# Kernel tuning notes

Hardware: AMD Instinct MI355X
Metric: run time of the kernel (lower is better)

Reference implementation:

```python
import jax, jax.numpy as jnp
import numpy as np

DIM = 1024
HEADS = 16
HEAD_DIM = DIM // HEADS
SCALE = HEAD_DIM ** -0.5
B, N = 2, 2048


def setup_inputs() -> dict:
    key = jax.random.key(0)
    ks = jax.random.split(key, 12)
    s = DIM ** -0.5
    return {
        "x_real": jax.random.normal(ks[0], (B, N, DIM), jnp.float32),
        "x_imag": jax.random.normal(ks[1], (B, N, DIM), jnp.float32),
        "Wqkv_r": jax.random.normal(ks[2], (3 * DIM, DIM), jnp.float32) * s,
        "bqkv_r": jax.random.normal(ks[3], (3 * DIM,), jnp.float32) * 0.01,
        "Wqkv_i": jax.random.normal(ks[4], (3 * DIM, DIM), jnp.float32) * s,
        "bqkv_i": jax.random.normal(ks[5], (3 * DIM,), jnp.float32) * 0.01,
        "Wout_r": jax.random.normal(ks[6], (DIM, DIM), jnp.float32) * s,
        "bout_r": jax.random.normal(ks[7], (DIM,), jnp.float32) * 0.01,
        "Wout_i": jax.random.normal(ks[8], (DIM, DIM), jnp.float32) * s,
        "bout_i": jax.random.normal(ks[9], (DIM,), jnp.float32) * 0.01,
    }


def _split_heads(qkv):
    # (B, N, 3*D) -> q, k, v each (B, H, N, hd)
    b, n, _ = qkv.shape
    qkv = qkv.reshape(b, n, 3, HEADS, HEAD_DIM).transpose(2, 0, 3, 1, 4)
    return qkv[0], qkv[1], qkv[2]


def reference(x_real, x_imag, Wqkv_r, bqkv_r, Wqkv_i, bqkv_i,
              Wout_r, bout_r, Wout_i, bout_i):
    b, n, d = x_real.shape
    q_r, k_r, v_r = _split_heads(x_real @ Wqkv_r.T + bqkv_r)
    q_i, k_i, v_i = _split_heads(x_imag @ Wqkv_i.T + bqkv_i)

    # complex score: (q_r + i q_i) (k_r - i k_i)^T pattern per source
    attn_real = (jnp.einsum('bhqd,bhkd->bhqk', q_r, k_r)
                 + jnp.einsum('bhqd,bhkd->bhqk', q_i, k_i)) * SCALE
    attn_imag = (jnp.einsum('bhqd,bhkd->bhqk', q_i, k_r)
                 - jnp.einsum('bhqd,bhkd->bhqk', q_r, k_i)) * SCALE
    attn_mag = jnp.sqrt(attn_real ** 2 + attn_imag ** 2)
    w = jax.nn.softmax(attn_mag, axis=-1)

    out_r = jnp.einsum('bhqk,bhkd->bhqd', w, v_r).transpose(0, 2, 1, 3).reshape(b, n, d)
    out_i = jnp.einsum('bhqk,bhkd->bhqd', w, v_i).transpose(0, 2, 1, 3).reshape(b, n, d)
    out_r = out_r @ Wout_r.T + bout_r
    out_i = out_i @ Wout_i.T + bout_i
    return out_r, out_i
```

## Files before the change

kernel.cpp:

```cpp
#include <hip/hip_runtime.h>


#define DIM_   1024
#define HEADS_ 16
#define HD_    64
#define BB_    2
#define NN_    2048
#define MTOT_  (BB_*NN_)
#define SCALE_ 0.125f

typedef __bf16 bf16;
typedef __bf16 bf16x8 __attribute__((ext_vector_type(8)));
typedef short  s16x8  __attribute__((ext_vector_type(8)));
typedef float  fx4    __attribute__((ext_vector_type(4)));

__device__ __forceinline__ bf16x8 neg8(bf16x8 v) {
    s16x8 s;
    __builtin_memcpy(&s, &v, sizeof(s));
    s ^= (short)0x8000;
    bf16x8 r;
    __builtin_memcpy(&r, &s, sizeof(r));
    return r;
}

__device__ __forceinline__ void gl_lds16(const void* g, void* l) {
    __builtin_amdgcn_global_load_lds(
        (const __attribute__((address_space(1))) unsigned int*)g,
        (__attribute__((address_space(3))) unsigned int*)l, 16, 0, 0);
}

#define PIPE_SYNC() asm volatile("s_waitcnt vmcnt(2)\n\ts_barrier" ::: "memory")

__global__ __launch_bounds__(256) void cvt_prepass(
    const float* __restrict__ xr, const float* __restrict__ xi,
    const float* __restrict__ wqr, const float* __restrict__ wqi,
    const float* __restrict__ wor, const float* __restrict__ woi,
    bf16* __restrict__ xbf, bf16* __restrict__ wqkv, bf16* __restrict__ wout)
{
    const int bid = blockIdx.x;
    const float* src; bf16* dst; int rel;
    if      (bid < 2048) { src = xr;  dst = xbf;           rel = bid; }
    else if (bid < 4096) { src = xi;  dst = xbf + 4194304; rel = bid - 2048; }
    else if (bid < 5632) { src = wqr; dst = wqkv;          rel = bid - 4096; }
    else if (bid < 7168) { src = wqi; dst = wqkv + 3145728; rel = bid - 5632; }
    else if (bid < 7680) { src = wor; dst = wout;          rel = bid - 7168; }
    else                 { src = woi; dst = wout + 1048576; rel = bid - 7680; }
    size_t base = (size_t)rel * 2048 + (size_t)threadIdx.x * 8;
    fx4 a = *(const fx4*)(src + base);
    fx4 b = *(const fx4*)(src + base + 4);
    bf16x8 o;
#pragma unroll
    for (int j = 0; j < 4; ++j) { o[j] = (bf16)a[j]; o[j+4] = (bf16)b[j]; }
    *(bf16x8*)(dst + base) = o;
}

#define GEMM_CORE(Aptr, Bptr)                                                  \
    __shared__ __align__(16) bf16 As[128*64];                                  \
    __shared__ __align__(16) bf16 Bs[128*64];                                  \
    const int tid  = threadIdx.x;                                              \
    const int w    = tid >> 6, lane = tid & 63;                                \
    const int quad = lane >> 4, lc = lane & 15;                                \
    const int wm   = (w >> 1) * 64, wn = (w & 1) * 64;                         \
    const int rj   = lane >> 3;                                                \
    const int sc   = (lane & 7) ^ rj;                                          \
    const fx4 fzero = {0.f, 0.f, 0.f, 0.f};                                    \
    fx4 acc[4][4];                                                             \
    _Pragma("unroll")                                                          \
    for (int mi = 0; mi < 4; ++mi)                                             \
        _Pragma("unroll")                                                      \
        for (int ni = 0; ni < 4; ++ni) acc[mi][ni] = fzero;                    \
    for (int k0 = 0; k0 < DIM_; k0 += 64) {                                    \
        _Pragma("unroll")                                                      \
        for (int j = 0; j < 4; ++j) {                                          \
            int grp = j*4 + w;                                                 \
            int gr  = grp*8 + rj;                                              \
            gl_lds16(Aptr + (size_t)(m0+gr)*DIM_ + k0 + sc*8, As + grp*512);   \
            gl_lds16(Bptr + (size_t)(n0+gr)*DIM_ + k0 + sc*8, Bs + grp*512);   \
        }                                                                      \
        __syncthreads();                                                       \
        bf16x8 af[2][4], bfr[2][4];                                            \
        _Pragma("unroll")                                                      \
        for (int ks = 0; ks < 2; ++ks) {                                       \
            _Pragma("unroll")                                                  \
            for (int mi = 0; mi < 4; ++mi)                                     \
                af[ks][mi] = *(bf16x8*)&As[(wm+mi*16+lc)*64 + (((ks*4+quad)^(lc&7))*8)]; \
            _Pragma("unroll")                                                  \
            for (int ni = 0; ni < 4; ++ni)                                     \
                bfr[ks][ni] = *(bf16x8*)&Bs[(wn+ni*16+lc)*64 + (((ks*4+quad)^(lc&7))*8)]; \
        }                                                                      \
        _Pragma("unroll")                                                      \
        for (int ks = 0; ks < 2; ++ks)                                         \
            _Pragma("unroll")                                                  \
            for (int mi = 0; mi < 4; ++mi)                                     \
                _Pragma("unroll")                                              \
                for (int ni = 0; ni < 4; ++ni)                                 \
                    acc[mi][ni] = __builtin_amdgcn_mfma_f32_16x16x32_bf16(     \
                        af[ks][mi], bfr[ks][ni], acc[mi][ni], 0, 0, 0);        \
        __syncthreads();                                                       \
    }

__global__ __launch_bounds__(256) void qkv_gemm_dma(
    const bf16* __restrict__ xbf, const bf16* __restrict__ wqkv,
    const float* __restrict__ br, const float* __restrict__ bi,
    bf16* __restrict__ qbuf, bf16* __restrict__ kbuf, bf16* __restrict__ vbuf)
{
    const int z = blockIdx.z;
    const bf16* __restrict__ Ap = xbf  + (size_t)z * 4194304;
    const bf16* __restrict__ Bp = wqkv + (size_t)z * 3145728;
    const float* __restrict__ bias = z ? bi : br;
    const int n0 = blockIdx.x * 128;
    const int m0 = blockIdx.y * 128;

    GEMM_CORE(Ap, Bp)

#pragma unroll
    for (int mi = 0; mi < 4; ++mi)
#pragma unroll
        for (int ni = 0; ni < 4; ++ni)
#pragma unroll
            for (int r = 0; r < 4; ++r) {
                int gm = m0 + wm + mi*16 + quad*4 + r;
                int gc = n0 + wn + ni*16 + lc;
                float val = acc[mi][ni][r] + bias[gc];
                bf16 bv = (bf16)val;
                int which = gc >> 10, h = (gc >> 6) & 15, hd = gc & 63;
                int b = gm >> 11, n = gm & 2047;
                size_t base = (size_t)((z*BB_ + b)*HEADS_ + h);
                if (which == 0)      qbuf[(base*NN_ + n)*HD_ + hd] = bv;
                else if (which == 1) kbuf[(base*NN_ + n)*HD_ + hd] = bv;
                else                 vbuf[(base*HD_ + hd)*NN_ + n] = bv;
            }
}

__global__ __launch_bounds__(256) void out_gemm_dma(
    const bf16* __restrict__ obuf, const bf16* __restrict__ wout,
    const float* __restrict__ br, const float* __restrict__ bi,
    float* __restrict__ out)
{
    const int z = blockIdx.z;
    const bf16* __restrict__ Ap = obuf + (size_t)z * 4194304;
    const bf16* __restrict__ Bp = wout + (size_t)z * 1048576;
    const float* __restrict__ bias = z ? bi : br;
    float* __restrict__ dst = out + (size_t)z * 4194304;
    const int n0 = blockIdx.x * 128;
    const int m0 = blockIdx.y * 128;

    GEMM_CORE(Ap, Bp)

#pragma unroll
    for (int mi = 0; mi < 4; ++mi)
#pragma unroll
        for (int ni = 0; ni < 4; ++ni)
#pragma unroll
            for (int r = 0; r < 4; ++r) {
                int gm = m0 + wm + mi*16 + quad*4 + r;
                int gc = n0 + wn + ni*16 + lc;
                dst[(size_t)gm*DIM_ + gc] = acc[mi][ni][r] + bias[gc];
            }
}

#define KT 32
#define NSTEP (NN_/KT)

__global__ __launch_bounds__(512, 4) void attn_fwd(
    const bf16* __restrict__ qbuf, const bf16* __restrict__ kbuf,
    const bf16* __restrict__ vbuf, bf16* __restrict__ obuf)
{
    const int bid = blockIdx.x;
    const int xcd = bid & 7;
    const int loc = bid >> 3;
    const int hb  = xcd*4 + (loc >> 4);
    const int blk = loc & 15;
    const int b = hb >> 4, h = hb & 15;

    const int tid  = threadIdx.x;
    const int w    = tid >> 6, lane = tid & 63;
    const int quad = lane >> 4, lc = lane & 15;
    const int q0   = blk*128 + w*16;

    __shared__ __align__(16) bf16 KV[3*8192];
    __shared__ __align__(16) bf16 Ps[8*16*40];
    bf16* psw = Ps + w*640;

    const size_t hR = (size_t)(b)*HEADS_ + h;
    const size_t hI = (size_t)(BB_ + b)*HEADS_ + h;
    const bf16* qrg = qbuf + hR*NN_*HD_;
    const bf16* qig = qbuf + hI*NN_*HD_;
    const char* krg = (const char*)(kbuf + hR*NN_*HD_);
    const char* kig = (const char*)(kbuf + hI*NN_*HD_);
    const char* vrg = (const char*)(vbuf + hR*HD_*NN_);
    const char* vig = (const char*)(vbuf + hI*HD_*NN_);

    const bf16* pr = qrg + (size_t)(q0 + lc)*HD_ + quad*8;
    const bf16* pi = qig + (size_t)(q0 + lc)*HD_ + quad*8;
    bf16x8 qr0 = *(const bf16x8*)(pr);
    bf16x8 qr1 = *(const bf16x8*)(pr + 32);
    bf16x8 qi0 = *(const bf16x8*)(pi);
    bf16x8 qi1 = *(const bf16x8*)(pi + 32);
    bf16x8 nqr0 = neg8(qr0), nqr1 = neg8(qr1);

    const int arr = w >> 1, half = w & 1;
    const char* stg_base = (arr == 0) ? krg : (arr == 1) ? kig
                         : (arr == 2) ? vrg : vig;
    size_t lane_off, step_mul, j_mul;
    if (arr < 2) {
        lane_off = (size_t)(lane >> 3)*128 + (size_t)((lane & 7) ^ (lane >> 3))*16;
        step_mul = 4096;  j_mul = 1024;
    } else {
        lane_off = (size_t)(lane >> 2)*4096 + (size_t)((lane & 3) ^ ((lane >> 3) & 3))*16;
        step_mul = 64;    j_mul = 65536;
    }
    const char* stg0 = stg_base + (size_t)half*2*j_mul + lane_off;
    const int lds_base = arr*2048 + half*1024;

    int koff[2][2], voff[4];
#pragma unroll
    for (int kb = 0; kb < 2; ++kb)
#pragma unroll
        for (int hf = 0; hf < 2; ++hf) {
            int r = kb*16 + lc;
            koff[kb][hf] = r*64 + (((hf*4 + quad) ^ (r & 7))*8);
        }
#pragma unroll
    for (int vb = 0; vb < 4; ++vb) {
        int r = vb*16 + lc;
        voff[vb] = r*32 + ((quad ^ ((r >> 1) & 3))*8);
    }

    const fx4 fzero = {0.f, 0.f, 0.f, 0.f};
    fx4 O[2][4];
    float l_[4];
#pragma unroll
    for (int r = 0; r < 4; ++r) l_[r] = 0.f;
#pragma unroll
    for (int ri = 0; ri < 2; ++ri)
#pragma unroll
        for (int vb = 0; vb < 4; ++vb) O[ri][vb] = fzero;
    bf16x8 pf;
    bf16x8 vf[2][4];

    const float CEXP = SCALE_ * 1.44269504f;

    {
        bf16* l = KV + lds_base;
        gl_lds16(stg0,          l);
        gl_lds16(stg0 + j_mul,  l + 512);
        l = KV + 8192 + lds_base;
        gl_lds16(stg0 + step_mul,         l);
        gl_lds16(stg0 + step_mul + j_mul, l + 512);
    }
    PIPE_SYNC();

    int b0 = 0, b1 = 8192, b2 = 16384;
    for (int s = 0; s < NSTEP; ++s) {
        if (s < NSTEP-2) {
            const char* g = stg0 + (size_t)(s+2)*step_mul;
            bf16* l = KV + b2 + lds_base;
            gl_lds16(g,         l);
            gl_lds16(g + j_mul, l + 512);
        }

        if (s > 0) {
#pragma unroll
            for (int ri = 0; ri < 2; ++ri)
#pragma unroll
                for (int vb = 0; vb < 4; ++vb)
                    O[ri][vb] = __builtin_amdgcn_mfma_f32_16x16x32_bf16(
                        pf, vf[ri][vb], O[ri][vb], 0, 0, 0);
        }

        bf16x8 kr_[2][2], ki_[2][2];
#pragma unroll
        for (int kb = 0; kb < 2; ++kb)
#pragma unroll
            for (int hf = 0; hf < 2; ++hf) {
                kr_[kb][hf] = *(bf16x8*)&KV[b0 + koff[kb][hf]];
                ki_[kb][hf] = *(bf16x8*)&KV[b0 + 2048 + koff[kb][hf]];
            }

#pragma unroll
        for (int kb = 0; kb < 2; ++kb) {
            fx4 sr = fzero, si = fzero;
            sr = __builtin_amdgcn_mfma_f32_16x16x32_bf16(qr0,  kr_[kb][0], sr, 0,0,0);
            sr = __builtin_amdgcn_mfma_f32_16x16x32_bf16(qr1,  kr_[kb][1], sr, 0,0,0);
            sr = __builtin_amdgcn_mfma_f32_16x16x32_bf16(qi0,  ki_[kb][0], sr, 0,0,0);
            sr = __builtin_amdgcn_mfma_f32_16x16x32_bf16(qi1,  ki_[kb][1], sr, 0,0,0);
            si = __builtin_amdgcn_mfma_f32_16x16x32_bf16(qi0,  kr_[kb][0], si, 0,0,0);
            si = __builtin_amdgcn_mfma_f32_16x16x32_bf16(qi1,  kr_[kb][1], si, 0,0,0);
            si = __builtin_amdgcn_mfma_f32_16x16x32_bf16(nqr0, ki_[kb][0], si, 0,0,0);
            si = __builtin_amdgcn_mfma_f32_16x16x32_bf16(nqr1, ki_[kb][1], si, 0,0,0);
#pragma unroll
            for (int r4 = 0; r4 < 4; ++r4) {
                float s2 = sr[r4]*sr[r4] + si[r4]*si[r4];
                float mg = __builtin_amdgcn_sqrtf(s2);
                float pv = __builtin_amdgcn_exp2f(mg * CEXP);
                l_[r4] += pv;
                psw[(quad*4 + r4)*40 + kb*16 + lc] = (bf16)pv;
            }
        }

        pf = *(bf16x8*)&psw[lc*40 + quad*8];
#pragma unroll
        for (int ri = 0; ri < 2; ++ri)
#pragma unroll
            for (int vb = 0; vb < 4; ++vb)
                vf[ri][vb] = *(bf16x8*)&KV[b0 + (2+ri)*2048 + voff[vb]];

        PIPE_SYNC();
        int t = b0; b0 = b1; b1 = b2; b2 = t;
    }

#pragma unroll
    for (int ri = 0; ri < 2; ++ri)
#pragma unroll
        for (int vb = 0; vb < 4; ++vb)
            O[ri][vb] = __builtin_amdgcn_mfma_f32_16x16x32_bf16(
                pf, vf[ri][vb], O[ri][vb], 0, 0, 0);

#pragma unroll
    for (int off = 1; off < 16; off <<= 1)
#pragma unroll
        for (int r = 0; r < 4; ++r)
            l_[r] += __shfl_xor(l_[r], off);
    float inv[4];
#pragma unroll
    for (int r = 0; r < 4; ++r) inv[r] = 1.f / l_[r];

    bf16* obr = obuf + ((size_t)(b)*NN_)*DIM_;
    bf16* obi = obuf + ((size_t)(BB_ + b)*NN_)*DIM_;
#pragma unroll
    for (int vb = 0; vb < 4; ++vb)
#pragma unroll
        for (int r = 0; r < 4; ++r) {
            int gn = q0 + quad*4 + r;
            int gc = h*HD_ + vb*16 + lc;
            obr[(size_t)gn*DIM_ + gc] = (bf16)(O[0][vb][r] * inv[r]);
            obi[(size_t)gn*DIM_ + gc] = (bf16)(O[1][vb][r] * inv[r]);
        }
}

__global__ __launch_bounds__(256) void qkv_gemm_legacy(
    const float* __restrict__ xr, const float* __restrict__ xi,
    const float* __restrict__ Wr, const float* __restrict__ Wi,
    const float* __restrict__ br, const float* __restrict__ bi,
    bf16* __restrict__ qbuf, bf16* __restrict__ kbuf, bf16* __restrict__ vbuf)
{
    const int z = blockIdx.z;
    const float* __restrict__ A    = z ? xi : xr;
    const float* __restrict__ W    = z ? Wi : Wr;
    const float* __restrict__ bias = z ? bi : br;
    const int n0 = blockIdx.x * 128;
    const int m0 = blockIdx.y * 128;

    __shared__ bf16 As[128*40];
    __shared__ bf16 Bs[128*40];

    const int tid  = threadIdx.x;
    const int w    = tid >> 6, lane = tid & 63;
    const int quad = lane >> 4, lc = lane & 15;
    const int wm   = (w >> 1) * 64, wn = (w & 1) * 64;

    const fx4 fzero = {0.f, 0.f, 0.f, 0.f};
    fx4 acc[4][4];
#pragma unroll
    for (int mi = 0; mi < 4; ++mi)
#pragma unroll
        for (int ni = 0; ni < 4; ++ni) acc[mi][ni] = fzero;

    for (int k0 = 0; k0 < DIM_; k0 += 32) {
#pragma unroll
        for (int it = 0; it < 2; ++it) {
            int flat = it*2048 + tid*8;
            int row = flat >> 5, col = flat & 31;
            const float* pa = A + (size_t)(m0+row)*DIM_ + k0 + col;
            const float* pb = W + (size_t)(n0+row)*DIM_ + k0 + col;
            fx4 a0 = *(const fx4*)pa, a1 = *(const fx4*)(pa+4);
            fx4 b0 = *(const fx4*)pb, b1 = *(const fx4*)(pb+4);
            bf16x8 av, bv;
#pragma unroll
            for (int j = 0; j < 4; ++j) {
                av[j] = (bf16)a0[j]; av[j+4] = (bf16)a1[j];
                bv[j] = (bf16)b0[j]; bv[j+4] = (bf16)b1[j];
            }
            *(bf16x8*)&As[row*40 + col] = av;
            *(bf16x8*)&Bs[row*40 + col] = bv;
        }
        __syncthreads();

        bf16x8 af[4], bfr[4];
#pragma unroll
        for (int mi = 0; mi < 4; ++mi) af[mi]  = *(bf16x8*)&As[(wm + mi*16 + lc)*40 + quad*8];
#pragma unroll
        for (int ni = 0; ni < 4; ++ni) bfr[ni] = *(bf16x8*)&Bs[(wn + ni*16 + lc)*40 + quad*8];
#pragma unroll
        for (int mi = 0; mi < 4; ++mi)
#pragma unroll
            for (int ni = 0; ni < 4; ++ni)
                acc[mi][ni] = __builtin_amdgcn_mfma_f32_16x16x32_bf16(af[mi], bfr[ni], acc[mi][ni], 0, 0, 0);
        __syncthreads();
    }

#pragma unroll
    for (int mi = 0; mi < 4; ++mi)
#pragma unroll
        for (int ni = 0; ni < 4; ++ni)
#pragma unroll
            for (int r = 0; r < 4; ++r) {
                int gm = m0 + wm + mi*16 + quad*4 + r;
                int gc = n0 + wn + ni*16 + lc;
                float val = acc[mi][ni][r] + bias[gc];
                bf16 bv = (bf16)val;
                int which = gc >> 10, h = (gc >> 6) & 15, hd = gc & 63;
                int b = gm >> 11, n = gm & 2047;
                size_t base = (size_t)((z*BB_ + b)*HEADS_ + h);
                if (which == 0)      qbuf[(base*NN_ + n)*HD_ + hd] = bv;
                else if (which == 1) kbuf[(base*NN_ + n)*HD_ + hd] = bv;
                else                 vbuf[(base*HD_ + hd)*NN_ + n] = bv;
            }
}

__global__ __launch_bounds__(256) void out_gemm_legacy(
    const bf16* __restrict__ obuf,
    const float* __restrict__ Wr, const float* __restrict__ Wi,
    const float* __restrict__ br, const float* __restrict__ bi,
    float* __restrict__ out)
{
    const int z = blockIdx.z;
    const bf16*  __restrict__ A    = obuf + (size_t)z * MTOT_ * DIM_;
    const float* __restrict__ W    = z ? Wi : Wr;
    const float* __restrict__ bias = z ? bi : br;
    float* __restrict__ dst        = out + (size_t)z * MTOT_ * DIM_;
    const int n0 = blockIdx.x * 128;
    const int m0 = blockIdx.y * 128;

    __shared__ bf16 As[128*40];
    __shared__ bf16 Bs[128*40];

    const int tid  = threadIdx.x;
    const int w    = tid >> 6, lane = tid & 63;
    const int quad = lane >> 4, lc = lane & 15;
    const int wm   = (w >> 1) * 64, wn = (w & 1) * 64;

    const fx4 fzero = {0.f, 0.f, 0.f, 0.f};
    fx4 acc[4][4];
#pragma unroll
    for (int mi = 0; mi < 4; ++mi)
#pragma unroll
        for (int ni = 0; ni < 4; ++ni) acc[mi][ni] = fzero;

    for (int k0 = 0; k0 < DIM_; k0 += 32) {
#pragma unroll
        for (int it = 0; it < 2; ++it) {
            int flat = it*2048 + tid*8;
            int row = flat >> 5, col = flat & 31;
            *(bf16x8*)&As[row*40 + col] = *(const bf16x8*)(A + (size_t)(m0+row)*DIM_ + k0 + col);
            const float* pb = W + (size_t)(n0+row)*DIM_ + k0 + col;
            fx4 b0 = *(const fx4*)pb, b1 = *(const fx4*)(pb+4);
            bf16x8 bv;
#pragma unroll
            for (int j = 0; j < 4; ++j) { bv[j] = (bf16)b0[j]; bv[j+4] = (bf16)b1[j]; }
            *(bf16x8*)&Bs[row*40 + col] = bv;
        }
        __syncthreads();

        bf16x8 af[4], bfr[4];
#pragma unroll
        for (int mi = 0; mi < 4; ++mi) af[mi]  = *(bf16x8*)&As[(wm + mi*16 + lc)*40 + quad*8];
#pragma unroll
        for (int ni = 0; ni < 4; ++ni) bfr[ni] = *(bf16x8*)&Bs[(wn + ni*16 + lc)*40 + quad*8];
#pragma unroll
        for (int mi = 0; mi < 4; ++mi)
#pragma unroll
            for (int ni = 0; ni < 4; ++ni)
                acc[mi][ni] = __builtin_amdgcn_mfma_f32_16x16x32_bf16(af[mi], bfr[ni], acc[mi][ni], 0, 0, 0);
        __syncthreads();
    }

#pragma unroll
    for (int mi = 0; mi < 4; ++mi)
#pragma unroll
        for (int ni = 0; ni < 4; ++ni)
#pragma unroll
            for (int r = 0; r < 4; ++r) {
                int gm = m0 + wm + mi*16 + quad*4 + r;
                int gc = n0 + wn + ni*16 + lc;
                dst[(size_t)gm*DIM_ + gc] = acc[mi][ni][r] + bias[gc];
            }
}

extern "C" void kernel_launch(void* const* d_in, const int* in_sizes, int n_in,
                              void* d_out, int out_size, void* d_ws, size_t ws_size,
                              hipStream_t stream) {
    const float* xr  = (const float*)d_in[0];
    const float* xi  = (const float*)d_in[1];
    const float* Wqr = (const float*)d_in[2];
    const float* bqr = (const float*)d_in[3];
    const float* Wqi = (const float*)d_in[4];
    const float* bqi = (const float*)d_in[5];
    const float* Wor = (const float*)d_in[6];
    const float* bor = (const float*)d_in[7];
    const float* Woi = (const float*)d_in[8];
    const float* boi = (const float*)d_in[9];
    float* out = (float*)d_out;

    bf16* ws = (bf16*)d_ws;
    const size_t NEED = 83886080ull;

    if (ws_size >= NEED) {
        bf16* xbf  = ws;
        bf16* wqkv = ws + 8388608;
        bf16* wout = ws + 14680064;
        bf16* qb   = ws + 16777216;
        bf16* kb   = ws + 25165824;
        bf16* vb   = ws + 33554432;
        bf16* obuf = xbf;

        cvt_prepass<<<dim3(8192), 256, 0, stream>>>(xr, xi, Wqr, Wqi, Wor, Woi,
                                                    xbf, wqkv, wout);
        qkv_gemm_dma<<<dim3(24, 32, 2), 256, 0, stream>>>(xbf, wqkv, bqr, bqi,
                                                          qb, kb, vb);
        attn_fwd<<<dim3(512), 512, 0, stream>>>(qb, kb, vb, obuf);
        out_gemm_dma<<<dim3(8, 32, 2), 256, 0, stream>>>(obuf, wout, bor, boi, out);
    } else {
        const size_t per = (size_t)2 * BB_ * HEADS_ * NN_ * HD_;
        bf16* qb   = ws;
        bf16* kb   = ws + per;
        bf16* vb   = ws + 2*per;
        bf16* obuf = ws + 3*per;
        qkv_gemm_legacy<<<dim3(24, 32, 2), 256, 0, stream>>>(xr, xi, Wqr, Wqi,
                                                             bqr, bqi, qb, kb, vb);
        attn_fwd<<<dim3(512), 512, 0, stream>>>(qb, kb, vb, obuf);
        out_gemm_legacy<<<dim3(8, 32, 2), 256, 0, stream>>>(obuf, Wor, Woi,
                                                            bor, boi, out);
    }
}
```

Baseline: 356.3 us.

## Transpose score MFMA to keep P in registers, drop LDS round-trip

Swaps the A/B operands of the QK^T MFMAs so each lane holds scores for one query row across eight keys. The probabilities can then be packed straight into the bf16x8 A-operand of the PV MFMA, with no write to and read back from shared memory. The K staging layout is permuted to match the new key order, and the row-sum reduction becomes a cross-quad shuffle plus a broadcast. This removes LDS traffic and a dependency stall per step, at the cost of a more intricate key-permutation mapping that must stay exactly consistent.

```diff
diff --git a/kernel.cpp b/kernel.cpp
--- a/kernel.cpp
+++ b/kernel.cpp
@@ -179,8 +179,6 @@
     const int q0   = blk*128 + w*16;
 
     __shared__ __align__(16) bf16 KV[3*8192];
-    __shared__ __align__(16) bf16 Ps[8*16*40];
-    bf16* psw = Ps + w*640;
 
     const size_t hR = (size_t)(b)*HEADS_ + h;
     const size_t hI = (size_t)(BB_ + b)*HEADS_ + h;
@@ -204,13 +202,16 @@
                          : (arr == 2) ? vrg : vig;
     size_t lane_off, step_mul, j_mul;
     if (arr < 2) {
-        lane_off = (size_t)(lane >> 3)*128 + (size_t)((lane & 7) ^ (lane >> 3))*16;
-        step_mul = 4096;  j_mul = 1024;
+        const int rl = lane >> 3;
+        const int p0 = (rl >> 2)*8 + half*4 + (rl & 3);
+        lane_off = (size_t)p0*128 + (size_t)((lane & 7) ^ rl)*16;
+        step_mul = 4096;  j_mul = 2048;
     } else {
-        lane_off = (size_t)(lane >> 2)*4096 + (size_t)((lane & 3) ^ ((lane >> 3) & 3))*16;
+        lane_off = (size_t)half*131072
+                 + (size_t)(lane >> 2)*4096 + (size_t)((lane & 3) ^ ((lane >> 3) & 3))*16;
         step_mul = 64;    j_mul = 65536;
     }
-    const char* stg0 = stg_base + (size_t)half*2*j_mul + lane_off;
+    const char* stg0 = stg_base + lane_off;
     const int lds_base = arr*2048 + half*1024;
 
     int koff[2][2], voff[4];
@@ -229,14 +230,12 @@
 
     const fx4 fzero = {0.f, 0.f, 0.f, 0.f};
     fx4 O[2][4];
-    float l_[4];
-#pragma unroll
-    for (int r = 0; r < 4; ++r) l_[r] = 0.f;
+    float l_ = 0.f;
 #pragma unroll
     for (int ri = 0; ri < 2; ++ri)
 #pragma unroll
         for (int vb = 0; vb < 4; ++vb) O[ri][vb] = fzero;
-    bf16x8 pf;
+    bf16x8 pf = {};
     bf16x8 vf[2][4];
 
     const float CEXP = SCALE_ * 1.44269504f;
@@ -281,25 +280,24 @@
 #pragma unroll
         for (int kb = 0; kb < 2; ++kb) {
             fx4 sr = fzero, si = fzero;
-            sr = __builtin_amdgcn_mfma_f32_16x16x32_bf16(qr0,  kr_[kb][0], sr, 0,0,0);
-            sr = __builtin_amdgcn_mfma_f32_16x16x32_bf16(qr1,  kr_[kb][1], sr, 0,0,0);
-            sr = __builtin_amdgcn_mfma_f32_16x16x32_bf16(qi0,  ki_[kb][0], sr, 0,0,0);
-            sr = __builtin_amdgcn_mfma_f32_16x16x32_bf16(qi1,  ki_[kb][1], sr, 0,0,0);
-            si = __builtin_amdgcn_mfma_f32_16x16x32_bf16(qi0,  kr_[kb][0], si, 0,0,0);
-            si = __builtin_amdgcn_mfma_f32_16x16x32_bf16(qi1,  kr_[kb][1], si, 0,0,0);
-            si = __builtin_amdgcn_mfma_f32_16x16x32_bf16(nqr0, ki_[kb][0], si, 0,0,0);
-            si = __builtin_amdgcn_mfma_f32_16x16x32_bf16(nqr1, ki_[kb][1], si, 0,0,0);
+            sr = __builtin_amdgcn_mfma_f32_16x16x32_bf16(kr_[kb][0], qr0,  sr, 0,0,0);
+            sr = __builtin_amdgcn_mfma_f32_16x16x32_bf16(kr_[kb][1], qr1,  sr, 0,0,0);
+            sr = __builtin_amdgcn_mfma_f32_16x16x32_bf16(ki_[kb][0], qi0,  sr, 0,0,0);
+            sr = __builtin_amdgcn_mfma_f32_16x16x32_bf16(ki_[kb][1], qi1,  sr, 0,0,0);
+            si = __builtin_amdgcn_mfma_f32_16x16x32_bf16(kr_[kb][0], qi0,  si, 0,0,0);
+            si = __builtin_amdgcn_mfma_f32_16x16x32_bf16(kr_[kb][1], qi1,  si, 0,0,0);
+            si = __builtin_amdgcn_mfma_f32_16x16x32_bf16(ki_[kb][0], nqr0, si, 0,0,0);
+            si = __builtin_amdgcn_mfma_f32_16x16x32_bf16(ki_[kb][1], nqr1, si, 0,0,0);
 #pragma unroll
             for (int r4 = 0; r4 < 4; ++r4) {
                 float s2 = sr[r4]*sr[r4] + si[r4]*si[r4];
                 float mg = __builtin_amdgcn_sqrtf(s2);
                 float pv = __builtin_amdgcn_exp2f(mg * CEXP);
-                l_[r4] += pv;
-                psw[(quad*4 + r4)*40 + kb*16 + lc] = (bf16)pv;
-            }
-        }
-
-        pf = *(bf16x8*)&psw[lc*40 + quad*8];
+                l_ += pv;
+                pf[kb*4 + r4] = (bf16)pv;
+            }
+        }
+
 #pragma unroll
         for (int ri = 0; ri < 2; ++ri)
 #pragma unroll
@@ -317,14 +315,11 @@
             O[ri][vb] = __builtin_amdgcn_mfma_f32_16x16x32_bf16(
                 pf, vf[ri][vb], O[ri][vb], 0, 0, 0);
 
-#pragma unroll
-    for (int off = 1; off < 16; off <<= 1)
-#pragma unroll
-        for (int r = 0; r < 4; ++r)
-            l_[r] += __shfl_xor(l_[r], off);
+    l_ += __shfl_xor(l_, 16);
+    l_ += __shfl_xor(l_, 32);
     float inv[4];
 #pragma unroll
-    for (int r = 0; r < 4; ++r) inv[r] = 1.f / l_[r];
+    for (int r = 0; r < 4; ++r) inv[r] = 1.f / __shfl(l_, quad*4 + r);
 
     bf16* obr = obuf + ((size_t)(b)*NN_)*DIM_;
     bf16* obi = obuf + ((size_t)(BB_ + b)*NN_)*DIM_;
```

Measured after the change: 337.5 us. 5.3% less time.
